# Performance work log

Measured on AMD Instinct MI355X. Metric: run time of the kernel, lower is better.

The kernel has to match this reference:

```python
import jax, jax.numpy as jnp
import numpy as np

BN_EPS = 1e-5

def setup_inputs() -> dict:
    key = jax.random.key(0)
    ks = jax.random.split(key, 12)
    B, C, H, W = 8, 512, 56, 56
    IC = 256  # inter_channels = in_channels // 2
    s_in = 1.0 / np.sqrt(C)
    s_ic = 1.0 / np.sqrt(IC)
    return {
        "x": jax.random.normal(ks[0], (B, C, H, W), dtype=jnp.float32),
        "theta_w": jax.random.normal(ks[1], (IC, C), dtype=jnp.float32) * s_in,
        "theta_b": jax.random.normal(ks[2], (IC,), dtype=jnp.float32) * s_in,
        "phi_w": jax.random.normal(ks[3], (IC, C), dtype=jnp.float32) * s_in,
        "phi_b": jax.random.normal(ks[4], (IC,), dtype=jnp.float32) * s_in,
        "g_w": jax.random.normal(ks[5], (IC, C), dtype=jnp.float32) * s_in,
        "g_b": jax.random.normal(ks[6], (IC,), dtype=jnp.float32) * s_in,
        "wz_w": jax.random.normal(ks[7], (C, IC), dtype=jnp.float32) * s_ic,
        "wz_b": jax.random.normal(ks[8], (C,), dtype=jnp.float32) * s_ic,
        "bn_w": jax.random.normal(ks[9], (C,), dtype=jnp.float32) * 0.1,
        "bn_b": jax.random.normal(ks[10], (C,), dtype=jnp.float32) * 0.1,
    }


def reference(x, theta_w, theta_b, phi_w, phi_b, g_w, g_b, wz_w, wz_b, bn_w, bn_b):
    B, C, H, W = x.shape
    N = H * W
    # [B, N, C] tokens
    xf = x.reshape(B, C, N).transpose(0, 2, 1)
    Q = jnp.einsum('bnc,ic->bni', xf, theta_w) + theta_b   # [B, N, IC]
    K = jnp.einsum('bnc,ic->bni', xf, phi_w) + phi_b       # [B, N, IC]
    V = jnp.einsum('bnc,ic->bni', xf, g_w) + g_b           # [B, N, IC]
    attn = jax.nn.softmax(jnp.einsum('bqi,bki->bqk', Q, K), axis=-1)  # [B, N, N]
    y = jnp.einsum('bqk,bki->bqi', attn, V)                # [B, N, IC]
    y = jnp.einsum('bqi,ci->bqc', y, wz_w) + wz_b          # [B, N, C]
    y = y.transpose(0, 2, 1).reshape(B, C, H, W)
    # BatchNorm2d, training-mode batch stats (biased variance)
    mean = jnp.mean(y, axis=(0, 2, 3))
    var = jnp.var(y, axis=(0, 2, 3))
    yn = (y - mean[None, :, None, None]) * jax.lax.rsqrt(var + BN_EPS)[None, :, None, None]
    y = yn * bn_w[None, :, None, None] + bn_b[None, :, None, None]
    return y + x
```

## Files before the change

### kernel.cpp

```cpp
#include <hip/hip_runtime.h>
#include <math.h>

#define B_  8
#define C_  512
#define N_  3136
#define IC_ 256

typedef __attribute__((ext_vector_type(8))) short bf16x8;
typedef __attribute__((ext_vector_type(4))) float f32x4;
typedef __attribute__((ext_vector_type(16))) float f32x16;

static __device__ __forceinline__ unsigned short f2bf(float f) {
    unsigned int u = __builtin_bit_cast(unsigned int, f);
    u = (u + 0x7fffu + ((u >> 16) & 1u)) >> 16;
    return (unsigned short)u;
}
static __device__ __forceinline__ float bf2f(unsigned short u) {
    return __builtin_bit_cast(float, (unsigned int)u << 16);
}
static __device__ __forceinline__ unsigned int pk2(float a, float b) {
    return (unsigned int)f2bf(a) | ((unsigned int)f2bf(b) << 16);
}

static __device__ __forceinline__ void gll16(const unsigned short* g, unsigned short* l) {
    __builtin_amdgcn_global_load_lds(
        (const __attribute__((address_space(1))) unsigned int*)g,
        (__attribute__((address_space(3))) unsigned int*)l, 16, 0, 0);
}

__global__ __launch_bounds__(256) void xpose_kernel(
    const float* __restrict__ x, unsigned short* __restrict__ xb)
{
    const int n0 = blockIdx.x * 64;
    const int c0 = blockIdx.y * 64;
    const int b  = blockIdx.z;
    __shared__ unsigned short T[64][72];
    const int tid = threadIdx.x;
#pragma unroll
    for (int e = 0; e < 4; ++e) {
        const int idx = tid + e * 256;
        const int row = idx >> 4;
        const int c4  = idx & 15;
        const float4 v = *(const float4*)&x[((size_t)b * C_ + c0 + row) * N_ + n0 + c4 * 4];
        T[c4 * 4 + 0][row] = f2bf(v.x);
        T[c4 * 4 + 1][row] = f2bf(v.y);
        T[c4 * 4 + 2][row] = f2bf(v.z);
        T[c4 * 4 + 3][row] = f2bf(v.w);
    }
    __syncthreads();
#pragma unroll
    for (int e = 0; e < 2; ++e) {
        const int s  = tid + e * 256;
        const int nr = s >> 3;
        const int sl = s & 7;
        *(bf16x8*)&xb[((size_t)b * N_ + n0 + nr) * C_ + c0 + sl * 8] =
            *(const bf16x8*)&T[nr][sl * 8];
    }
}

__global__ __launch_bounds__(256) void wconv_kernel(
    const float* __restrict__ tw, const float* __restrict__ pw,
    const float* __restrict__ gw, const float* __restrict__ wzw,
    unsigned short* __restrict__ Wcat, unsigned short* __restrict__ wzwb)
{
    const int gid = blockIdx.x * 256 + threadIdx.x;
    if (gid < 98304) {
        const int i  = gid >> 7;
        const int c4 = gid & 127;
        const float* src = (i < 256) ? &tw[(size_t)i * 512]
                         : (i < 512) ? &pw[(size_t)(i - 256) * 512]
                                     : &gw[(size_t)(i - 512) * 512];
        const float4 v = *(const float4*)&src[c4 * 4];
        ushort4 o; o.x = f2bf(v.x); o.y = f2bf(v.y); o.z = f2bf(v.z); o.w = f2bf(v.w);
        *(ushort4*)&Wcat[(size_t)i * 512 + c4 * 4] = o;
    } else {
        const int g2 = gid - 98304;
        const int r  = g2 >> 6;
        const int c4 = g2 & 63;
        const float4 v = *(const float4*)&wzw[(size_t)r * 256 + c4 * 4];
        ushort4 o; o.x = f2bf(v.x); o.y = f2bf(v.y); o.z = f2bf(v.z); o.w = f2bf(v.w);
        *(ushort4*)&wzwb[(size_t)r * 256 + c4 * 4] = o;
    }
}

__global__ __launch_bounds__(256, 2) void qkv_mfma_kernel(
    const unsigned short* __restrict__ xb, const unsigned short* __restrict__ Wcat,
    const float* __restrict__ tb, const float* __restrict__ pb,
    const float* __restrict__ gb,
    unsigned short* __restrict__ Q, unsigned short* __restrict__ K,
    unsigned short* __restrict__ Vt)
{
    const int n0 = blockIdx.x * 64;
    const int by = blockIdx.y;
    const int b  = blockIdx.z;
    const int i0 = by * 128;
    const int tid = threadIdx.x;
    const int wq = tid >> 6, lane = tid & 63;
    const int g = lane >> 4, c = lane & 15;
    const int wm = wq >> 1, wn = wq & 1;

    __shared__ unsigned short smem[12288];
    unsigned short* Asm = smem;
    unsigned short* Bsm = smem + 4096;

    const int srow = tid >> 3;
    const int ssl  = tid & 7;

    f32x4 acc[2][4];
#pragma unroll
    for (int mb = 0; mb < 2; ++mb)
#pragma unroll
        for (int nb = 0; nb < 4; ++nb) acc[mb][nb] = (f32x4){0.f, 0.f, 0.f, 0.f};

    bf16x8 ast[2], bst[4];
#pragma unroll
    for (int e = 0; e < 2; ++e) {
        const int row = srow + e * 32;
        ast[e] = *(const bf16x8*)&xb[((size_t)b * N_ + n0 + row) * C_ + ((ssl ^ (row & 7)) << 3)];
    }
#pragma unroll
    for (int e = 0; e < 4; ++e) {
        const int row = srow + e * 32;
        bst[e] = *(const bf16x8*)&Wcat[(size_t)(i0 + row) * C_ + ((ssl ^ (row & 7)) << 3)];
    }
#pragma unroll
    for (int e = 0; e < 2; ++e) *(bf16x8*)&Asm[(srow + e * 32) * 64 + ssl * 8] = ast[e];
#pragma unroll
    for (int e = 0; e < 4; ++e) *(bf16x8*)&Bsm[(srow + e * 32) * 64 + ssl * 8] = bst[e];
    __syncthreads();

    const int arow[2] = { wm * 32 + c, wm * 32 + 16 + c };
    const int brow[4] = { wn * 64 + c, wn * 64 + 16 + c, wn * 64 + 32 + c, wn * 64 + 48 + c };

    for (int s = 0; s < 8; ++s) {
        const int c0n = (s < 7) ? (s + 1) * 64 : s * 64;
#pragma unroll
        for (int e = 0; e < 2; ++e) {
            const int row = srow + e * 32;
            ast[e] = *(const bf16x8*)&xb[((size_t)b * N_ + n0 + row) * C_ + c0n + ((ssl ^ (row & 7)) << 3)];
        }
#pragma unroll
        for (int e = 0; e < 4; ++e) {
            const int row = srow + e * 32;
            bst[e] = *(const bf16x8*)&Wcat[(size_t)(i0 + row) * C_ + c0n + ((ssl ^ (row & 7)) << 3)];
        }
#pragma unroll
        for (int ks = 0; ks < 2; ++ks) {
            bf16x8 af[2], bfr[4];
            const int sl = ((ks << 2) | g);
#pragma unroll
            for (int mb = 0; mb < 2; ++mb)
                af[mb] = *(const bf16x8*)&Asm[arow[mb] * 64 + ((sl ^ (c & 7)) << 3)];
#pragma unroll
            for (int nb = 0; nb < 4; ++nb)
                bfr[nb] = *(const bf16x8*)&Bsm[brow[nb] * 64 + ((sl ^ (c & 7)) << 3)];
#pragma unroll
            for (int mb = 0; mb < 2; ++mb)
#pragma unroll
                for (int nb = 0; nb < 4; ++nb)
                    acc[mb][nb] = __builtin_amdgcn_mfma_f32_16x16x32_bf16(af[mb], bfr[nb], acc[mb][nb], 0, 0, 0);
        }
        __syncthreads();
#pragma unroll
        for (int e = 0; e < 2; ++e) *(bf16x8*)&Asm[(srow + e * 32) * 64 + ssl * 8] = ast[e];
#pragma unroll
        for (int e = 0; e < 4; ++e) *(bf16x8*)&Bsm[(srow + e * 32) * 64 + ssl * 8] = bst[e];
        __syncthreads();
    }

    const int proj = by >> 1;
    const float* bias = (proj == 0) ? tb : (proj == 1) ? pb : gb;
    const int icb = (by & 1) * 128;
    if (proj < 2) {
        unsigned short* out = (proj == 0) ? Q : K;
#pragma unroll
        for (int mb = 0; mb < 2; ++mb)
#pragma unroll
            for (int nb = 0; nb < 4; ++nb)
#pragma unroll
                for (int r = 0; r < 4; ++r) {
                    const int token = n0 + wm * 32 + mb * 16 + g * 4 + r;
                    const int ic = icb + wn * 64 + nb * 16 + c;
                    out[((size_t)b * N_ + token) * IC_ + ic] = f2bf(acc[mb][nb][r] + bias[ic]);
                }
    } else {
        unsigned short* T = smem;
#pragma unroll
        for (int mb = 0; mb < 2; ++mb)
#pragma unroll
            for (int nb = 0; nb < 4; ++nb)
#pragma unroll
                for (int r = 0; r < 4; ++r) {
                    const int il = wn * 64 + nb * 16 + c;
                    const int tl = wm * 32 + mb * 16 + g * 4 + r;
                    T[il * 72 + tl] = f2bf(acc[mb][nb][r] + bias[icb + il]);
                }
        __syncthreads();
#pragma unroll
        for (int e = 0; e < 4; ++e) {
            const int row = (tid >> 3) + e * 32;
            *(bf16x8*)&Vt[((size_t)b * IC_ + icb + row) * N_ + n0 + ((tid & 7) * 8)] =
                *(const bf16x8*)&T[row * 72 + (tid & 7) * 8];
        }
    }
}

__global__ __launch_bounds__(512, 2) void attn_kernel(
    const unsigned short* __restrict__ Q, const unsigned short* __restrict__ K,
    const unsigned short* __restrict__ Vt,
    unsigned short* __restrict__ part, float2* __restrict__ ml)
{
    const int b     = blockIdx.x;
    const int qb    = blockIdx.y;
    const int split = blockIdx.z;
    int q0 = qb * 256; if (q0 > N_ - 256) q0 = N_ - 256;
    const int t0 = split ? 25 : 0;
    const int t1 = split ? 49 : 25;

    const int tid  = threadIdx.x;
    const int wq   = tid >> 6;
    const int lane = tid & 63;
    const int ql   = lane & 31;
    const int h    = lane >> 5;

    const unsigned short* Qb = Q  + (size_t)b * N_ * IC_;
    const unsigned short* Kb = K  + (size_t)b * N_ * IC_;
    const unsigned short* Vb = Vt + (size_t)b * IC_ * N_;

    __shared__ unsigned short Ks[2][64 * 256];
    __shared__ unsigned short Vs[2][256 * 64];

    const int krow = tid >> 5, ksl = tid & 31;
    const int vrow = tid >> 3, vsl = tid & 7;
    const unsigned short* kg = Kb + (size_t)krow * IC_ + ((ksl ^ (krow & 7)) << 3);
    const unsigned short* vg = Vb + (size_t)vrow * N_ + ((vsl ^ (vrow & 7)) << 3);

#define STAGE(buf, t)                                                          \
    {                                                                          \
        const unsigned short* kgp = kg + (size_t)(t) * 64 * IC_;               \
        const unsigned short* vgp = vg + (size_t)(t) * 64;                     \
        _Pragma("unroll") for (int e = 0; e < 4; ++e)                          \
            gll16(kgp + (size_t)e * 16 * IC_, &Ks[buf][(tid + e * 512) * 8]);  \
        _Pragma("unroll") for (int e = 0; e < 4; ++e)                          \
            gll16(vgp + (size_t)e * 64 * N_, &Vs[buf][(tid + e * 512) * 8]);   \
    }

    bf16x8 qf[16];
    {
        const unsigned short* qrow = &Qb[(size_t)(q0 + wq * 32 + ql) * IC_ + h * 8];
#pragma unroll
        for (int s = 0; s < 16; ++s) qf[s] = *(const bf16x8*)&qrow[s * 16];
    }

    f32x16 yacc[8];
#pragma unroll
    for (int db = 0; db < 8; ++db)
#pragma unroll
        for (int i = 0; i < 16; ++i) yacc[db][i] = 0.f;
    float m = -1e30f, lsum = 0.f;

    STAGE(0, t0);
    asm volatile("s_waitcnt vmcnt(0)" ::: "memory");
    __syncthreads();

    for (int t = t0; t < t1; ++t) {
        const int cur = (t - t0) & 1;
        if (t + 1 < t1) STAGE(cur ^ 1, t + 1);

        f32x16 s0, s1;
#pragma unroll
        for (int i = 0; i < 16; ++i) { s0[i] = 0.f; s1[i] = 0.f; }
        __builtin_amdgcn_s_setprio(1);
#pragma unroll
        for (int s = 0; s < 16; ++s) {
            const int sl = ((2 * s + h) ^ (ql & 7)) << 3;
            const bf16x8 kf0 = *(const bf16x8*)&Ks[cur][(size_t)ql * 256 + sl];
            s0 = __builtin_amdgcn_mfma_f32_32x32x16_bf16(kf0, qf[s], s0, 0, 0, 0);
            const bf16x8 kf1 = *(const bf16x8*)&Ks[cur][(size_t)(32 + ql) * 256 + sl];
            s1 = __builtin_amdgcn_mfma_f32_32x32x16_bf16(kf1, qf[s], s1, 0, 0, 0);
        }
        __builtin_amdgcn_s_setprio(0);

        float mx[16];
#pragma unroll
        for (int i = 0; i < 16; ++i) mx[i] = fmaxf(s0[i], s1[i]);
#pragma unroll
        for (int off = 8; off > 0; off >>= 1)
#pragma unroll
            for (int i = 0; i < 8; ++i)
                if (i < off) mx[i] = fmaxf(mx[i], mx[i + off]);
        float rm = fmaxf(mx[0], __shfl_xor(mx[0], 32));

        if (__any(rm > m + 8.f)) {
            const float mnew  = fmaxf(m, rm);
            const float scale = __expf(m - mnew);
            m = mnew;
            lsum *= scale;
#pragma unroll
            for (int db = 0; db < 8; ++db)
#pragma unroll
                for (int i = 0; i < 16; ++i) yacc[db][i] *= scale;
        }

#pragma unroll
        for (int i = 0; i < 16; ++i) s0[i] = __expf(s0[i] - m);
#pragma unroll
        for (int i = 0; i < 16; ++i) s1[i] = __expf(s1[i] - m);
        float sm[16];
#pragma unroll
        for (int i = 0; i < 16; ++i) sm[i] = s0[i] + s1[i];
#pragma unroll
        for (int off = 8; off > 0; off >>= 1)
#pragma unroll
            for (int i = 0; i < 8; ++i)
                if (i < off) sm[i] += sm[i + off];
        lsum += sm[0] + __shfl_xor(sm[0], 32);

        unsigned int pk0[8], pk1[8];
#pragma unroll
        for (int w = 0; w < 8; ++w) {
            pk0[w] = pk2(s0[2 * w], s0[2 * w + 1]);
            pk1[w] = pk2(s1[2 * w], s1[2 * w + 1]);
        }

#pragma unroll
        for (int s = 0; s < 4; ++s) {
            const unsigned int* u4 = (s >> 1) ? &pk1[4 * (s & 1)] : &pk0[4 * (s & 1)];
            const unsigned int send0 = h ? u4[0] : u4[2];
            const unsigned int send1 = h ? u4[1] : u4[3];
            const unsigned int r0 = (unsigned int)__shfl_xor((int)send0, 32);
            const unsigned int r1 = (unsigned int)__shfl_xor((int)send1, 32);
            uint4 fw;
            fw.x = h ? r0 : u4[0];
            fw.y = h ? r1 : u4[1];
            fw.z = h ? u4[2] : r0;
            fw.w = h ? u4[3] : r1;
            const bf16x8 pf = __builtin_bit_cast(bf16x8, fw);
            const int vsl_r = ((2 * s + h) ^ (ql & 7)) << 3;
            __builtin_amdgcn_s_setprio(1);
#pragma unroll
            for (int db = 0; db < 8; ++db) {
                const bf16x8 vf =
                    *(const bf16x8*)&Vs[cur][(size_t)(db * 32 + ql) * 64 + vsl_r];
                yacc[db] = __builtin_amdgcn_mfma_f32_32x32x16_bf16(vf, pf, yacc[db], 0, 0, 0);
            }
            __builtin_amdgcn_s_setprio(0);
        }

        asm volatile("s_waitcnt vmcnt(0)" ::: "memory");
        __syncthreads();
    }

    const size_t pbase = (size_t)(b * 2 + split) * N_;
    const int q = q0 + wq * 32 + ql;
    if (h == 0) ml[pbase + q] = make_float2(m, lsum);
#pragma unroll
    for (int db = 0; db < 8; ++db)
#pragma unroll
        for (int rq = 0; rq < 4; ++rq) {
            ushort4 o;
            o.x = f2bf(yacc[db][4 * rq + 0]);
            o.y = f2bf(yacc[db][4 * rq + 1]);
            o.z = f2bf(yacc[db][4 * rq + 2]);
            o.w = f2bf(yacc[db][4 * rq + 3]);
            *(ushort4*)&part[(pbase + q) * IC_ + 32 * db + 8 * rq + 4 * h] = o;
        }
#undef STAGE
}

__global__ __launch_bounds__(256) void attn_merge_kernel(
    const unsigned short* __restrict__ part, const float2* __restrict__ ml,
    unsigned short* __restrict__ Y)
{
    const int b  = blockIdx.y;
    const int q  = blockIdx.x * 64 + (threadIdx.x >> 2);
    const int d0 = (threadIdx.x & 3) * 64;
    const float2 A  = ml[(size_t)(b * 2 + 0) * N_ + q];
    const float2 Bv = ml[(size_t)(b * 2 + 1) * N_ + q];
    const float mm = fmaxf(A.x, Bv.x);
    const float wA = __expf(A.x - mm), wB = __expf(Bv.x - mm);
    const float inv = 1.f / (A.y * wA + Bv.y * wB);
    const unsigned short* pA = &part[((size_t)(b * 2 + 0) * N_ + q) * IC_ + d0];
    const unsigned short* pB = &part[((size_t)(b * 2 + 1) * N_ + q) * IC_ + d0];
    unsigned short* y = &Y[((size_t)b * N_ + q) * IC_ + d0];
#pragma unroll
    for (int j = 0; j < 8; ++j) {
        const bf16x8 va = *(const bf16x8*)&pA[j * 8];
        const bf16x8 vb = *(const bf16x8*)&pB[j * 8];
        unsigned short o[8];
#pragma unroll
        for (int k = 0; k < 8; ++k)
            o[k] = f2bf((bf2f((unsigned short)va[k]) * wA +
                         bf2f((unsigned short)vb[k]) * wB) * inv);
        *(bf16x8*)&y[j * 8] = *(const bf16x8*)o;
    }
}

__global__ __launch_bounds__(256, 2) void wz_mfma_kernel(
    const unsigned short* __restrict__ Yb, const unsigned short* __restrict__ wzwb,
    const float* __restrict__ wzb, float* __restrict__ Z)
{
    const int n0 = blockIdx.x * 64;
    const int c0 = blockIdx.y * 128;
    const int b  = blockIdx.z;
    const int tid = threadIdx.x;
    const int wq = tid >> 6, lane = tid & 63;
    const int g = lane >> 4, c = lane & 15;
    const int wm = wq >> 1, wn = wq & 1;

    __shared__ unsigned short smem[12288];
    unsigned short* Asm = smem;
    unsigned short* Bsm = smem + 8192;

    const int srow = tid >> 3;
    const int ssl  = tid & 7;

    f32x4 acc[4][2];
#pragma unroll
    for (int mb = 0; mb < 4; ++mb)
#pragma unroll
        for (int nb = 0; nb < 2; ++nb) acc[mb][nb] = (f32x4){0.f, 0.f, 0.f, 0.f};

    bf16x8 ast[4], bst[2];
#pragma unroll
    for (int e = 0; e < 4; ++e) {
        const int row = srow + e * 32;
        ast[e] = *(const bf16x8*)&wzwb[(size_t)(c0 + row) * IC_ + ((ssl ^ (row & 7)) << 3)];
    }
#pragma unroll
    for (int e = 0; e < 2; ++e) {
        const int row = srow + e * 32;
        bst[e] = *(const bf16x8*)&Yb[((size_t)b * N_ + n0 + row) * IC_ + ((ssl ^ (row & 7)) << 3)];
    }
#pragma unroll
    for (int e = 0; e < 4; ++e) *(bf16x8*)&Asm[(srow + e * 32) * 64 + ssl * 8] = ast[e];
#pragma unroll
    for (int e = 0; e < 2; ++e) *(bf16x8*)&Bsm[(srow + e * 32) * 64 + ssl * 8] = bst[e];
    __syncthreads();

    const int arow[4] = { wm * 64 + c, wm * 64 + 16 + c, wm * 64 + 32 + c, wm * 64 + 48 + c };
    const int brow[2] = { wn * 32 + c, wn * 32 + 16 + c };

    for (int s = 0; s < 4; ++s) {
        const int k0n = (s < 3) ? (s + 1) * 64 : s * 64;
#pragma unroll
        for (int e = 0; e < 4; ++e) {
            const int row = srow + e * 32;
            ast[e] = *(const bf16x8*)&wzwb[(size_t)(c0 + row) * IC_ + k0n + ((ssl ^ (row & 7)) << 3)];
        }
#pragma unroll
        for (int e = 0; e < 2; ++e) {
            const int row = srow + e * 32;
            bst[e] = *(const bf16x8*)&Yb[((size_t)b * N_ + n0 + row) * IC_ + k0n + ((ssl ^ (row & 7)) << 3)];
        }
#pragma unroll
        for (int ks = 0; ks < 2; ++ks) {
            bf16x8 af[4], bfr[2];
            const int sl = ((ks << 2) | g);
#pragma unroll
            for (int mb = 0; mb < 4; ++mb)
                af[mb] = *(const bf16x8*)&Asm[arow[mb] * 64 + ((sl ^ (c & 7)) << 3)];
#pragma unroll
            for (int nb = 0; nb < 2; ++nb)
                bfr[nb] = *(const bf16x8*)&Bsm[brow[nb] * 64 + ((sl ^ (c & 7)) << 3)];
#pragma unroll
            for (int mb = 0; mb < 4; ++mb)
#pragma unroll
                for (int nb = 0; nb < 2; ++nb)
                    acc[mb][nb] = __builtin_amdgcn_mfma_f32_16x16x32_bf16(af[mb], bfr[nb], acc[mb][nb], 0, 0, 0);
        }
        __syncthreads();
#pragma unroll
        for (int e = 0; e < 4; ++e) *(bf16x8*)&Asm[(srow + e * 32) * 64 + ssl * 8] = ast[e];
#pragma unroll
        for (int e = 0; e < 2; ++e) *(bf16x8*)&Bsm[(srow + e * 32) * 64 + ssl * 8] = bst[e];
        __syncthreads();
    }

#pragma unroll
    for (int mb = 0; mb < 4; ++mb) {
#pragma unroll
        for (int r = 0; r < 4; ++r) {
            const int cg = c0 + wm * 64 + mb * 16 + g * 4 + r;
            const float bw = wzb[cg];
#pragma unroll
            for (int nb = 0; nb < 2; ++nb) {
                const int ng = n0 + wn * 32 + nb * 16 + c;
                Z[((size_t)b * C_ + cg) * N_ + ng] = acc[mb][nb][r] + bw;
            }
        }
    }
}

__global__ __launch_bounds__(256) void bn_stats_kernel(
    const float* __restrict__ Z, float* __restrict__ stats)
{
    const int c   = blockIdx.x;
    const int tid = threadIdx.x;
    double s = 0.0, s2 = 0.0;
    for (int b = 0; b < B_; ++b) {
        const float* p = Z + ((size_t)b * C_ + c) * N_;
        for (int n = tid; n < N_; n += 256) {
            const double v = (double)p[n];
            s += v; s2 += v * v;
        }
    }
    __shared__ double ls[256], ls2[256];
    ls[tid] = s; ls2[tid] = s2;
    __syncthreads();
    for (int off = 128; off > 0; off >>= 1) {
        if (tid < off) { ls[tid] += ls[tid + off]; ls2[tid] += ls2[tid + off]; }
        __syncthreads();
    }
    if (tid == 0) {
        const double M    = (double)B_ * (double)N_;
        const double mean = ls[0] / M;
        const double var  = ls2[0] / M - mean * mean;
        stats[c]      = (float)mean;
        stats[C_ + c] = (float)var;
    }
}

__global__ __launch_bounds__(256) void bn_apply_kernel(
    const float* __restrict__ Z, const float* __restrict__ x,
    const float* __restrict__ stats,
    const float* __restrict__ bnw, const float* __restrict__ bnb,
    float* __restrict__ out)
{
    const size_t total4 = (size_t)B_ * C_ * N_ / 4;
    const size_t i4 = (size_t)blockIdx.x * blockDim.x + threadIdx.x;
    if (i4 >= total4) return;
    const size_t i = i4 * 4;
    const int c = (int)((i / N_) % C_);
    const float mean = stats[c];
    const float var  = stats[C_ + c];
    const float sc = rsqrtf(var + 1e-5f) * bnw[c];
    const float sh = bnb[c] - mean * sc;
    const float4 z  = ((const float4*)Z)[i4];
    const float4 xv = ((const float4*)x)[i4];
    float4 o;
    o.x = z.x * sc + sh + xv.x;
    o.y = z.y * sc + sh + xv.y;
    o.z = z.z * sc + sh + xv.z;
    o.w = z.w * sc + sh + xv.w;
    ((float4*)out)[i4] = o;
}

extern "C" void kernel_launch(void* const* d_in, const int* in_sizes, int n_in,
                              void* d_out, int out_size, void* d_ws, size_t ws_size,
                              hipStream_t stream)
{
    const float* x   = (const float*)d_in[0];
    const float* tw  = (const float*)d_in[1];
    const float* tb  = (const float*)d_in[2];
    const float* pw  = (const float*)d_in[3];
    const float* pb  = (const float*)d_in[4];
    const float* gw  = (const float*)d_in[5];
    const float* gb  = (const float*)d_in[6];
    const float* wzw = (const float*)d_in[7];
    const float* wzb = (const float*)d_in[8];
    const float* bnw = (const float*)d_in[9];
    const float* bnb = (const float*)d_in[10];
    float* out = (float*)d_out;

    const size_t NIC = (size_t)B_ * N_ * IC_;
    const size_t BNC = (size_t)B_ * N_ * C_;
    unsigned short* Qw   = (unsigned short*)d_ws;
    unsigned short* Kw   = Qw + NIC;
    unsigned short* Vtw  = Kw + NIC;
    unsigned short* Ybw  = Vtw + NIC;
    unsigned short* xbw  = Ybw + NIC;
    unsigned short* partw = xbw;
    unsigned short* Wcat = xbw + BNC;
    unsigned short* wzwb = Wcat + 768 * 512;
    float* stats = (float*)(wzwb + 512 * 256);
    float2* mlw  = (float2*)(stats + 2 * C_);
    float* Zb    = out;

    wconv_kernel<<<512, 256, 0, stream>>>(tw, pw, gw, wzw, Wcat, wzwb);
    xpose_kernel<<<dim3(N_ / 64, C_ / 64, B_), 256, 0, stream>>>(x, xbw);
    qkv_mfma_kernel<<<dim3(N_ / 64, 6, B_), 256, 0, stream>>>(
        xbw, Wcat, tb, pb, gb, Qw, Kw, Vtw);
    attn_kernel<<<dim3(B_, 13, 2), 512, 0, stream>>>(Qw, Kw, Vtw, partw, mlw);
    attn_merge_kernel<<<dim3(N_ / 64, B_), 256, 0, stream>>>(partw, mlw, Ybw);
    wz_mfma_kernel<<<dim3(N_ / 64, C_ / 128, B_), 256, 0, stream>>>(Ybw, wzwb, wzb, Zb);
    bn_stats_kernel<<<C_, 256, 0, stream>>>(Zb, stats);
    const int total4 = B_ * C_ * N_ / 4;
    bn_apply_kernel<<<(total4 + 255) / 256, 256, 0, stream>>>(Zb, x, stats, bnw, bnb, out);
}
```

Baseline: 290.4 us.

## Fuse BN partial stats into Wz epilogue and widen attention LDS swizzle

```diff
diff --git a/kernel.cpp b/kernel.cpp
--- a/kernel.cpp
+++ b/kernel.cpp
@@ -5,6 +5,7 @@
 #define C_  512
 #define N_  3136
 #define IC_ 256
+#define NPART 784
 
 typedef __attribute__((ext_vector_type(8))) short bf16x8;
 typedef __attribute__((ext_vector_type(4))) float f32x4;
@@ -222,6 +223,7 @@
     const int lane = tid & 63;
     const int ql   = lane & 31;
     const int h    = lane >> 5;
+    const int swz0 = (ql & 7) ^ (ql >> 3);
 
     const unsigned short* Qb = Q  + (size_t)b * N_ * IC_;
     const unsigned short* Kb = K  + (size_t)b * N_ * IC_;
@@ -232,17 +234,20 @@
 
     const int krow = tid >> 5, ksl = tid & 31;
     const int vrow = tid >> 3, vsl = tid & 7;
-    const unsigned short* kg = Kb + (size_t)krow * IC_ + ((ksl ^ (krow & 7)) << 3);
-    const unsigned short* vg = Vb + (size_t)vrow * N_ + ((vsl ^ (vrow & 7)) << 3);
-
-#define STAGE(buf, t)                                                          \
-    {                                                                          \
-        const unsigned short* kgp = kg + (size_t)(t) * 64 * IC_;               \
-        const unsigned short* vgp = vg + (size_t)(t) * 64;                     \
-        _Pragma("unroll") for (int e = 0; e < 4; ++e)                          \
-            gll16(kgp + (size_t)e * 16 * IC_, &Ks[buf][(tid + e * 512) * 8]);  \
-        _Pragma("unroll") for (int e = 0; e < 4; ++e)                          \
-            gll16(vgp + (size_t)e * 64 * N_, &Vs[buf][(tid + e * 512) * 8]);   \
+    const unsigned short* vg =
+        Vb + (size_t)vrow * N_ + ((vsl ^ ((vrow & 7) ^ ((vrow >> 3) & 7))) << 3);
+
+#define STAGE(buf, t)                                                            \
+    {                                                                            \
+        _Pragma("unroll") for (int e = 0; e < 4; ++e) {                          \
+            const int kr = krow + e * 16;                                        \
+            gll16(Kb + ((size_t)(t) * 64 + kr) * IC_ +                           \
+                      ((ksl ^ ((kr & 7) ^ ((kr >> 3) & 7))) << 3),               \
+                  &Ks[buf][(tid + e * 512) * 8]);                                \
+        }                                                                        \
+        const unsigned short* vgp = vg + (size_t)(t) * 64;                       \
+        _Pragma("unroll") for (int e = 0; e < 4; ++e)                            \
+            gll16(vgp + (size_t)e * 64 * N_, &Vs[buf][(tid + e * 512) * 8]);     \
     }
 
     bf16x8 qf[16];
@@ -273,10 +278,10 @@
         __builtin_amdgcn_s_setprio(1);
 #pragma unroll
         for (int s = 0; s < 16; ++s) {
-            const int sl = ((2 * s + h) ^ (ql & 7)) << 3;
+            const int sl = ((2 * s + h) ^ swz0) << 3;
             const bf16x8 kf0 = *(const bf16x8*)&Ks[cur][(size_t)ql * 256 + sl];
             s0 = __builtin_amdgcn_mfma_f32_32x32x16_bf16(kf0, qf[s], s0, 0, 0, 0);
-            const bf16x8 kf1 = *(const bf16x8*)&Ks[cur][(size_t)(32 + ql) * 256 + sl];
+            const bf16x8 kf1 = *(const bf16x8*)&Ks[cur][(size_t)(32 + ql) * 256 + (sl ^ 32)];
             s1 = __builtin_amdgcn_mfma_f32_32x32x16_bf16(kf1, qf[s], s1, 0, 0, 0);
         }
         __builtin_amdgcn_s_setprio(0);
@@ -336,12 +341,12 @@
             fw.z = h ? u4[2] : r0;
             fw.w = h ? u4[3] : r1;
             const bf16x8 pf = __builtin_bit_cast(bf16x8, fw);
-            const int vsl_r = ((2 * s + h) ^ (ql & 7)) << 3;
+            const int vsl_r = ((2 * s + h) ^ swz0) << 3;
             __builtin_amdgcn_s_setprio(1);
 #pragma unroll
             for (int db = 0; db < 8; ++db) {
-                const bf16x8 vf =
-                    *(const bf16x8*)&Vs[cur][(size_t)(db * 32 + ql) * 64 + vsl_r];
+                const bf16x8 vf = *(const bf16x8*)
+                    &Vs[cur][(size_t)(db * 32 + ql) * 64 + (vsl_r ^ (((db & 1) << 2) << 3))];
                 yacc[db] = __builtin_amdgcn_mfma_f32_32x32x16_bf16(vf, pf, yacc[db], 0, 0, 0);
             }
             __builtin_amdgcn_s_setprio(0);
@@ -398,7 +403,8 @@
 
 __global__ __launch_bounds__(256, 2) void wz_mfma_kernel(
     const unsigned short* __restrict__ Yb, const unsigned short* __restrict__ wzwb,
-    const float* __restrict__ wzb, float* __restrict__ Z)
+    const float* __restrict__ wzb, float* __restrict__ Z,
+    float2* __restrict__ partial)
 {
     const int n0 = blockIdx.x * 64;
     const int c0 = blockIdx.y * 128;
@@ -477,45 +483,50 @@
         __syncthreads();
     }
 
+    const int slot = (b * 49 + blockIdx.x) * 2 + wn;
 #pragma unroll
     for (int mb = 0; mb < 4; ++mb) {
 #pragma unroll
         for (int r = 0; r < 4; ++r) {
             const int cg = c0 + wm * 64 + mb * 16 + g * 4 + r;
             const float bw = wzb[cg];
-#pragma unroll
-            for (int nb = 0; nb < 2; ++nb) {
-                const int ng = n0 + wn * 32 + nb * 16 + c;
-                Z[((size_t)b * C_ + cg) * N_ + ng] = acc[mb][nb][r] + bw;
+            const float z0 = acc[mb][0][r] + bw;
+            const float z1 = acc[mb][1][r] + bw;
+            Z[((size_t)b * C_ + cg) * N_ + n0 + wn * 32 + c]      = z0;
+            Z[((size_t)b * C_ + cg) * N_ + n0 + wn * 32 + 16 + c] = z1;
+            float ps = z0 + z1;
+            float pq = z0 * z0 + z1 * z1;
+#pragma unroll
+            for (int off = 1; off <= 8; off <<= 1) {
+                ps += __shfl_xor(ps, off);
+                pq += __shfl_xor(pq, off);
             }
-        }
-    }
-}
-
-__global__ __launch_bounds__(256) void bn_stats_kernel(
-    const float* __restrict__ Z, float* __restrict__ stats)
+            if (c == 0) partial[(size_t)cg * NPART + slot] = make_float2(ps, pq);
+        }
+    }
+}
+
+__global__ __launch_bounds__(256) void bn_finalize_kernel(
+    const float2* __restrict__ partial, float* __restrict__ stats)
 {
     const int c   = blockIdx.x;
     const int tid = threadIdx.x;
-    double s = 0.0, s2 = 0.0;
-    for (int b = 0; b < B_; ++b) {
-        const float* p = Z + ((size_t)b * C_ + c) * N_;
-        for (int n = tid; n < N_; n += 256) {
-            const double v = (double)p[n];
-            s += v; s2 += v * v;
-        }
-    }
-    __shared__ double ls[256], ls2[256];
-    ls[tid] = s; ls2[tid] = s2;
+    double s = 0.0, q = 0.0;
+    for (int i = tid; i < NPART; i += 256) {
+        const float2 p = partial[(size_t)c * NPART + i];
+        s += p.x; q += p.y;
+    }
+    __shared__ double ls[256], lq[256];
+    ls[tid] = s; lq[tid] = q;
     __syncthreads();
     for (int off = 128; off > 0; off >>= 1) {
-        if (tid < off) { ls[tid] += ls[tid + off]; ls2[tid] += ls2[tid + off]; }
+        if (tid < off) { ls[tid] += ls[tid + off]; lq[tid] += lq[tid + off]; }
         __syncthreads();
     }
     if (tid == 0) {
         const double M    = (double)B_ * (double)N_;
         const double mean = ls[0] / M;
-        const double var  = ls2[0] / M - mean * mean;
+        const double var  = lq[0] / M - mean * mean;
         stats[c]      = (float)mean;
         stats[C_ + c] = (float)var;
     }
@@ -575,6 +586,7 @@
     unsigned short* wzwb = Wcat + 768 * 512;
     float* stats = (float*)(wzwb + 512 * 256);
     float2* mlw  = (float2*)(stats + 2 * C_);
+    float2* bnpart = mlw + (size_t)B_ * 2 * N_;
     float* Zb    = out;
 
     wconv_kernel<<<512, 256, 0, stream>>>(tw, pw, gw, wzw, Wcat, wzwb);
@@ -583,8 +595,8 @@
         xbw, Wcat, tb, pb, gb, Qw, Kw, Vtw);
     attn_kernel<<<dim3(B_, 13, 2), 512, 0, stream>>>(Qw, Kw, Vtw, partw, mlw);
     attn_merge_kernel<<<dim3(N_ / 64, B_), 256, 0, stream>>>(partw, mlw, Ybw);
-    wz_mfma_kernel<<<dim3(N_ / 64, C_ / 128, B_), 256, 0, stream>>>(Ybw, wzwb, wzb, Zb);
-    bn_stats_kernel<<<C_, 256, 0, stream>>>(Zb, stats);
+    wz_mfma_kernel<<<dim3(N_ / 64, C_ / 128, B_), 256, 0, stream>>>(Ybw, wzwb, wzb, Zb, bnpart);
+    bn_finalize_kernel<<<C_, 256, 0, stream>>>(bnpart, stats);
     const int total4 = B_ * C_ * N_ / 4;
     bn_apply_kernel<<<(total4 + 255) / 256, 256, 0, stream>>>(Zb, x, stats, bnw, bnb, out);
 }
```

Result: faster. 273.2 us, median of 2 (-5.9%).
